# Kernel tuning notes

Hardware: AMD Instinct MI355X
Metric: run time of the kernel (lower is better)

Reference implementation:

```python
import jax, jax.numpy as jnp
import numpy as np

EPS = 1e-12  # matches F.normalize default eps

def _angle(e):
    # e: [N, D] embeddings
    d = e[:, None, :] - e[None, :, :]                      # [N, N, D] pairwise differences
    n = jnp.linalg.norm(d, axis=-1, keepdims=True)         # [N, N, 1]
    d = d / jnp.maximum(n, EPS)                            # normalized diffs; diagonal stays 0
    # all-triplet cosines: for each anchor i, Gram matrix of its normalized diffs
    return jnp.einsum('ijd,ikd->ijk', d, d)                # [N, N, N]

def _smooth_l1_mean(a, b):
    # torch F.smooth_l1_loss with beta=1.0, reduction='mean'
    x = jnp.abs(a - b)
    return jnp.mean(jnp.where(x < 1.0, 0.5 * x * x, x - 0.5))

def setup_inputs() -> dict:
    key = jax.random.key(0)
    k1, k2 = jax.random.split(key)
    student = jax.random.normal(k1, (384, 256), dtype=jnp.float32)
    teacher = jax.random.normal(k2, (384, 256), dtype=jnp.float32)
    return {"student": student, "teacher": teacher}

def reference(student, teacher):
    s_angle = _angle(student)
    t_angle = _angle(teacher)
    return _smooth_l1_mean(s_angle, t_angle)
```

## Files before the change

kernel.cpp:

```cpp
#include <hip/hip_runtime.h>
#include <hip/hip_bf16.h>

#define NPTS 384
#define IT 16
#define NZI (NPTS/IT)
#define DIMS 256

__global__ __launch_bounds__(256) void gram_kernel(
        const float* __restrict__ Es, const float* __restrict__ Et,
        float* __restrict__ Gs, float* __restrict__ Gt,
        float2* __restrict__ UHs, float2* __restrict__ UHt,
        float* __restrict__ out) {
    const int z = blockIdx.z;
    const float* __restrict__ E  = z ? Et : Es;
    float*       __restrict__ G  = z ? Gt : Gs;
    float2*      __restrict__ UH = z ? UHt : UHs;

    const int tx = threadIdx.x;
    const int ty = threadIdx.y;
    const int t  = ty * 16 + tx;
    const int i0 = blockIdx.x * 32;
    const int j0 = blockIdx.y * 32;

    if (blockIdx.x == 0 && blockIdx.y == 0 && z == 0 && t == 0) out[0] = 0.0f;

    __shared__ float sn[64];
    {
        const int r = t >> 2;
        const int p = t & 3;
        const int row = (r < 32) ? (i0 + r) : (j0 + r - 32);
        const float4* __restrict__ src = (const float4*)(E + row * DIMS) + p * 16;
        float s = 0.f;
#pragma unroll
        for (int k = 0; k < 16; k++) {
            float4 v = src[k];
            s += v.x * v.x + v.y * v.y + v.z * v.z + v.w * v.w;
        }
        s += __shfl_xor(s, 1, 64);
        s += __shfl_xor(s, 2, 64);
        if (p == 0) sn[r] = s;
    }
    __syncthreads();

    const int i = i0 + 2 * ty;
    const int j = j0 + 2 * tx;
    const float4* __restrict__ a0 = (const float4*)(E + i * DIMS);
    const float4* __restrict__ a1 = (const float4*)(E + (i + 1) * DIMS);
    const float4* __restrict__ b0 = (const float4*)(E + j * DIMS);
    const float4* __restrict__ b1 = (const float4*)(E + (j + 1) * DIMS);

    float g00 = 0.f, g01 = 0.f, g10 = 0.f, g11 = 0.f;
#pragma unroll 8
    for (int k = 0; k < DIMS / 4; k++) {
        float4 av0 = a0[k], av1 = a1[k], bv0 = b0[k], bv1 = b1[k];
        g00 = fmaf(av0.x, bv0.x, g00); g00 = fmaf(av0.y, bv0.y, g00);
        g00 = fmaf(av0.z, bv0.z, g00); g00 = fmaf(av0.w, bv0.w, g00);
        g01 = fmaf(av0.x, bv1.x, g01); g01 = fmaf(av0.y, bv1.y, g01);
        g01 = fmaf(av0.z, bv1.z, g01); g01 = fmaf(av0.w, bv1.w, g01);
        g10 = fmaf(av1.x, bv0.x, g10); g10 = fmaf(av1.y, bv0.y, g10);
        g10 = fmaf(av1.z, bv0.z, g10); g10 = fmaf(av1.w, bv0.w, g10);
        g11 = fmaf(av1.x, bv1.x, g11); g11 = fmaf(av1.y, bv1.y, g11);
        g11 = fmaf(av1.z, bv1.z, g11); g11 = fmaf(av1.w, bv1.w, g11);
    }

    const float g[2][2] = {{g00, g01}, {g10, g11}};
    const float si[2] = {sn[2 * ty], sn[2 * ty + 1]};
    const float sj[2] = {sn[32 + 2 * tx], sn[32 + 2 * tx + 1]};
#pragma unroll
    for (int r = 0; r < 2; r++) {
#pragma unroll
        for (int c = 0; c < 2; c++) {
            const int ii = i + r, jj = j + c;
            const float gv = g[r][c];
            const float v  = si[r] + sj[c] - 2.0f * gv;
            const float n  = sqrtf(fmaxf(v, 0.0f));
            const float u  = (ii == jj) ? 0.0f : (1.0f / fmaxf(n, 1e-12f));
            G[ii * NPTS + jj]  = gv;
            UH[ii * NPTS + jj] = make_float2(u, 0.5f * si[r] - gv);
        }
    }
}

__global__ __launch_bounds__(256) void rkd_main_kernel(
        const float* __restrict__ Gs, const float* __restrict__ Gt,
        const float2* __restrict__ UHs, const float2* __restrict__ UHt,
        float* __restrict__ out) {
    const int tlin = blockIdx.x;
    const int kt = (int)((sqrtf(8.0f * (float)tlin + 1.0f) - 1.0f) * 0.5f);
    const int jt = tlin - (kt * (kt + 1)) / 2;

    const int tx = threadIdx.x;
    const int ty = threadIdx.y;
    const int jb = jt * 64 + 4 * ty;
    const int kb = kt * 64 + 4 * tx;
    const int ibase = blockIdx.y * IT;

    float wh[4][4];
    const bool offd = (jt != kt);
#pragma unroll
    for (int a = 0; a < 4; a++)
#pragma unroll
        for (int b = 0; b < 4; b++) {
            const int jj = jb + a, kk = kb + b;
            const float w2 = offd ? 2.0f : (kk > jj ? 2.0f : (kk == jj ? 1.0f : 0.0f));
            wh[a][b] = 0.5f * w2;
        }

    float gs[4][4], gt[4][4];
#pragma unroll
    for (int a = 0; a < 4; a++) {
        const float4 vs = *(const float4*)(Gs + (jb + a) * NPTS + kb);
        const float4 vt = *(const float4*)(Gt + (jb + a) * NPTS + kb);
        gs[a][0] = vs.x; gs[a][1] = vs.y; gs[a][2] = vs.z; gs[a][3] = vs.w;
        gt[a][0] = vt.x; gt[a][1] = vt.y; gt[a][2] = vt.z; gt[a][3] = vt.w;
    }

    const float4* __restrict__ pjs = (const float4*)(UHs + (size_t)ibase * NPTS + jb);
    const float4* __restrict__ pjt = (const float4*)(UHt + (size_t)ibase * NPTS + jb);
    const float4* __restrict__ pks = (const float4*)(UHs + (size_t)ibase * NPTS + kb);
    const float4* __restrict__ pkt = (const float4*)(UHt + (size_t)ibase * NPTS + kb);

    float acc = 0.0f;
#pragma unroll 2
    for (int iz = 0; iz < IT; iz++) {
        const int ro = iz * (NPTS / 2);
        const float4 js0 = pjs[ro], js1 = pjs[ro + 1];
        const float4 jt0 = pjt[ro], jt1 = pjt[ro + 1];
        const float4 ks0 = pks[ro], ks1 = pks[ro + 1];
        const float4 kt0 = pkt[ro], kt1 = pkt[ro + 1];

        const float u_sj[4] = {js0.x, js0.z, js1.x, js1.z};
        const float h_sj[4] = {js0.y, js0.w, js1.y, js1.w};
        const float u_tj[4] = {jt0.x, jt0.z, jt1.x, jt1.z};
        const float h_tj[4] = {jt0.y, jt0.w, jt1.y, jt1.w};
        const float u_sk[4] = {ks0.x, ks0.z, ks1.x, ks1.z};
        const float h_sk[4] = {ks0.y, ks0.w, ks1.y, ks1.w};
        const float u_tk[4] = {kt0.x, kt0.z, kt1.x, kt1.z};
        const float h_tk[4] = {kt0.y, kt0.w, kt1.y, kt1.w};

#pragma unroll
        for (int a = 0; a < 4; a++) {
            const float usa = u_sj[a], hsa = h_sj[a];
            const float uta = u_tj[a], hta = h_tj[a];
#pragma unroll
            for (int b = 0; b < 4; b++) {
                const float ts = gs[a][b] + hsa + h_sk[b];
                const float tt = gt[a][b] + hta + h_tk[b];
                const float ps = usa * u_sk[b];
                const float pt = uta * u_tk[b];
                const float mt = pt * tt;
                const float d  = fmaf(ps, ts, -mt);
                const float q  = d * d;
                const float w  = fmaf(2.0f, fabsf(d), -1.0f);
                const float l  = __builtin_amdgcn_fmed3f(q, w, 1.0f);
                acc = fmaf(wh[a][b], l, acc);
            }
        }
    }

#pragma unroll
    for (int off = 32; off > 0; off >>= 1)
        acc += __shfl_down(acc, off, 64);

    __shared__ float wsum[4];
    const int tid  = ty * 16 + tx;
    const int wid  = tid >> 6;
    const int lane = tid & 63;
    if (lane == 0) wsum[wid] = acc;
    __syncthreads();
    if (tid == 0) {
        const float s = wsum[0] + wsum[1] + wsum[2] + wsum[3];
        atomicAdd(out, s * (1.0f / (384.0f * 384.0f * 384.0f)));
    }
}

extern "C" void kernel_launch(void* const* d_in, const int* in_sizes, int n_in,
                              void* d_out, int out_size, void* d_ws, size_t ws_size,
                              hipStream_t stream) {
    const float* student = (const float*)d_in[0];
    const float* teacher = (const float*)d_in[1];
    float* out = (float*)d_out;

    float*  Gs  = (float*)d_ws;
    float*  Gt  = Gs + NPTS * NPTS;
    float2* UHs = (float2*)(Gt + NPTS * NPTS);
    float2* UHt = UHs + NPTS * NPTS;

    gram_kernel<<<dim3(NPTS / 32, NPTS / 32, 2), dim3(16, 16), 0, stream>>>(
        student, teacher, Gs, Gt, UHs, UHt, out);

    rkd_main_kernel<<<dim3(21, NZI), dim3(16, 16), 0, stream>>>(
        Gs, Gt, UHs, UHt, out);
}
```

Baseline: 114.9 us.

## Split Gram computation over K, add derive pass, prefetch and branch main loop

The Gram kernel is split four ways along the feature dimension into partial buffers, and a new elementwise kernel sums the partials and derives norms, inverse distances and half-terms. This raises parallelism in the first stage at the cost of an extra launch and extra workspace traffic. The main kernel halves the i-tile so it launches more blocks, software-prefetches the next row of UH values into registers, and drops the per-element weight multiply on off-diagonal tiles. It also sets occupancy hints through launch_bounds.

New measurement: 109.2 us. -4.9%, faster.

```diff
diff --git a/kernel.cpp b/kernel.cpp
--- a/kernel.cpp
+++ b/kernel.cpp
@@ -2,57 +2,35 @@
 #include <hip/hip_bf16.h>
 
 #define NPTS 384
-#define IT 16
-#define NZI (NPTS/IT)
+#define NN (NPTS * NPTS)
 #define DIMS 256
-
-__global__ __launch_bounds__(256) void gram_kernel(
+#define KSPLIT 4
+#define KCH (DIMS / KSPLIT)
+#define IT 8
+#define NZI (NPTS / IT)
+
+__global__ __launch_bounds__(256, 4) void gram_part_kernel(
         const float* __restrict__ Es, const float* __restrict__ Et,
-        float* __restrict__ Gs, float* __restrict__ Gt,
-        float2* __restrict__ UHs, float2* __restrict__ UHt,
-        float* __restrict__ out) {
-    const int z = blockIdx.z;
-    const float* __restrict__ E  = z ? Et : Es;
-    float*       __restrict__ G  = z ? Gt : Gs;
-    float2*      __restrict__ UH = z ? UHt : UHs;
+        float* __restrict__ P) {
+    const int m  = blockIdx.z >> 2;
+    const int kc = (blockIdx.z & 3) * KCH;
+    const float* __restrict__ E = m ? Et : Es;
+    float* __restrict__ Gp = P + (size_t)blockIdx.z * NN;
 
     const int tx = threadIdx.x;
     const int ty = threadIdx.y;
-    const int t  = ty * 16 + tx;
-    const int i0 = blockIdx.x * 32;
-    const int j0 = blockIdx.y * 32;
-
-    if (blockIdx.x == 0 && blockIdx.y == 0 && z == 0 && t == 0) out[0] = 0.0f;
-
-    __shared__ float sn[64];
-    {
-        const int r = t >> 2;
-        const int p = t & 3;
-        const int row = (r < 32) ? (i0 + r) : (j0 + r - 32);
-        const float4* __restrict__ src = (const float4*)(E + row * DIMS) + p * 16;
-        float s = 0.f;
-#pragma unroll
-        for (int k = 0; k < 16; k++) {
-            float4 v = src[k];
-            s += v.x * v.x + v.y * v.y + v.z * v.z + v.w * v.w;
-        }
-        s += __shfl_xor(s, 1, 64);
-        s += __shfl_xor(s, 2, 64);
-        if (p == 0) sn[r] = s;
-    }
-    __syncthreads();
-
-    const int i = i0 + 2 * ty;
-    const int j = j0 + 2 * tx;
-    const float4* __restrict__ a0 = (const float4*)(E + i * DIMS);
-    const float4* __restrict__ a1 = (const float4*)(E + (i + 1) * DIMS);
-    const float4* __restrict__ b0 = (const float4*)(E + j * DIMS);
-    const float4* __restrict__ b1 = (const float4*)(E + (j + 1) * DIMS);
+    const int i  = blockIdx.x * 32 + 2 * ty;
+    const int j  = blockIdx.y * 32 + 2 * tx;
+
+    const float4* __restrict__ a0 = (const float4*)(E + i * DIMS + kc);
+    const float4* __restrict__ a1 = (const float4*)(E + (i + 1) * DIMS + kc);
+    const float4* __restrict__ b0 = (const float4*)(E + j * DIMS + kc);
+    const float4* __restrict__ b1 = (const float4*)(E + (j + 1) * DIMS + kc);
 
     float g00 = 0.f, g01 = 0.f, g10 = 0.f, g11 = 0.f;
-#pragma unroll 8
-    for (int k = 0; k < DIMS / 4; k++) {
-        float4 av0 = a0[k], av1 = a1[k], bv0 = b0[k], bv1 = b1[k];
+#pragma unroll
+    for (int k = 0; k < KCH / 4; k++) {
+        const float4 av0 = a0[k], av1 = a1[k], bv0 = b0[k], bv1 = b1[k];
         g00 = fmaf(av0.x, bv0.x, g00); g00 = fmaf(av0.y, bv0.y, g00);
         g00 = fmaf(av0.z, bv0.z, g00); g00 = fmaf(av0.w, bv0.w, g00);
         g01 = fmaf(av0.x, bv1.x, g01); g01 = fmaf(av0.y, bv1.y, g01);
@@ -63,25 +41,39 @@
         g11 = fmaf(av1.z, bv1.z, g11); g11 = fmaf(av1.w, bv1.w, g11);
     }
 
-    const float g[2][2] = {{g00, g01}, {g10, g11}};
-    const float si[2] = {sn[2 * ty], sn[2 * ty + 1]};
-    const float sj[2] = {sn[32 + 2 * tx], sn[32 + 2 * tx + 1]};
-#pragma unroll
-    for (int r = 0; r < 2; r++) {
-#pragma unroll
-        for (int c = 0; c < 2; c++) {
-            const int ii = i + r, jj = j + c;
-            const float gv = g[r][c];
-            const float v  = si[r] + sj[c] - 2.0f * gv;
-            const float n  = sqrtf(fmaxf(v, 0.0f));
-            const float u  = (ii == jj) ? 0.0f : (1.0f / fmaxf(n, 1e-12f));
-            G[ii * NPTS + jj]  = gv;
-            UH[ii * NPTS + jj] = make_float2(u, 0.5f * si[r] - gv);
-        }
-    }
-}
-
-__global__ __launch_bounds__(256) void rkd_main_kernel(
+    *(float2*)(Gp + i * NPTS + j)       = make_float2(g00, g01);
+    *(float2*)(Gp + (i + 1) * NPTS + j) = make_float2(g10, g11);
+}
+
+__global__ __launch_bounds__(256, 4) void derive_kernel(
+        const float* __restrict__ P,
+        float* __restrict__ Gs, float* __restrict__ Gt,
+        float2* __restrict__ UHs, float2* __restrict__ UHt,
+        float* __restrict__ out) {
+    const int idx = blockIdx.x * 256 + threadIdx.x;
+    if (idx == 0) out[0] = 0.0f;
+    const int z   = idx / NN;
+    const int rem = idx - z * NN;
+    const int i   = rem / NPTS;
+    const int j   = rem - i * NPTS;
+
+    const float* __restrict__ bz = P + (size_t)z * 4 * NN;
+    const int di = i * (NPTS + 1);
+    const int dj = j * (NPTS + 1);
+
+    const float g   = bz[rem] + bz[NN + rem] + bz[2 * NN + rem] + bz[3 * NN + rem];
+    const float gii = bz[di]  + bz[NN + di]  + bz[2 * NN + di]  + bz[3 * NN + di];
+    const float gjj = bz[dj]  + bz[NN + dj]  + bz[2 * NN + dj]  + bz[3 * NN + dj];
+
+    const float v = gii + gjj - 2.0f * g;
+    const float n = sqrtf(fmaxf(v, 0.0f));
+    const float u = (i == j) ? 0.0f : (1.0f / fmaxf(n, 1e-12f));
+
+    (z ? Gt : Gs)[rem]   = g;
+    (z ? UHt : UHs)[rem] = make_float2(u, 0.5f * gii - g);
+}
+
+__global__ __launch_bounds__(256, 3) void rkd_main_kernel(
         const float* __restrict__ Gs, const float* __restrict__ Gt,
         const float2* __restrict__ UHs, const float2* __restrict__ UHt,
         float* __restrict__ out) {
@@ -95,17 +87,6 @@
     const int kb = kt * 64 + 4 * tx;
     const int ibase = blockIdx.y * IT;
 
-    float wh[4][4];
-    const bool offd = (jt != kt);
-#pragma unroll
-    for (int a = 0; a < 4; a++)
-#pragma unroll
-        for (int b = 0; b < 4; b++) {
-            const int jj = jb + a, kk = kb + b;
-            const float w2 = offd ? 2.0f : (kk > jj ? 2.0f : (kk == jj ? 1.0f : 0.0f));
-            wh[a][b] = 0.5f * w2;
-        }
-
     float gs[4][4], gt[4][4];
 #pragma unroll
     for (int a = 0; a < 4; a++) {
@@ -120,42 +101,83 @@
     const float4* __restrict__ pks = (const float4*)(UHs + (size_t)ibase * NPTS + kb);
     const float4* __restrict__ pkt = (const float4*)(UHt + (size_t)ibase * NPTS + kb);
 
+    const bool offd = (jt != kt);
+    float wh[4][4];
+#pragma unroll
+    for (int a = 0; a < 4; a++)
+#pragma unroll
+        for (int b = 0; b < 4; b++) {
+            const int jj = jb + a, kk = kb + b;
+            wh[a][b] = (kk > jj) ? 1.0f : ((kk == jj) ? 0.5f : 0.0f);
+        }
+
+    float4 L[8];
+    L[0] = pjs[0]; L[1] = pjs[1];
+    L[2] = pjt[0]; L[3] = pjt[1];
+    L[4] = pks[0]; L[5] = pks[1];
+    L[6] = pkt[0]; L[7] = pkt[1];
+
     float acc = 0.0f;
 #pragma unroll 2
     for (int iz = 0; iz < IT; iz++) {
-        const int ro = iz * (NPTS / 2);
-        const float4 js0 = pjs[ro], js1 = pjs[ro + 1];
-        const float4 jt0 = pjt[ro], jt1 = pjt[ro + 1];
-        const float4 ks0 = pks[ro], ks1 = pks[ro + 1];
-        const float4 kt0 = pkt[ro], kt1 = pkt[ro + 1];
-
-        const float u_sj[4] = {js0.x, js0.z, js1.x, js1.z};
-        const float h_sj[4] = {js0.y, js0.w, js1.y, js1.w};
-        const float u_tj[4] = {jt0.x, jt0.z, jt1.x, jt1.z};
-        const float h_tj[4] = {jt0.y, jt0.w, jt1.y, jt1.w};
-        const float u_sk[4] = {ks0.x, ks0.z, ks1.x, ks1.z};
-        const float h_sk[4] = {ks0.y, ks0.w, ks1.y, ks1.w};
-        const float u_tk[4] = {kt0.x, kt0.z, kt1.x, kt1.z};
-        const float h_tk[4] = {kt0.y, kt0.w, kt1.y, kt1.w};
-
-#pragma unroll
-        for (int a = 0; a < 4; a++) {
-            const float usa = u_sj[a], hsa = h_sj[a];
-            const float uta = u_tj[a], hta = h_tj[a];
-#pragma unroll
-            for (int b = 0; b < 4; b++) {
-                const float ts = gs[a][b] + hsa + h_sk[b];
-                const float tt = gt[a][b] + hta + h_tk[b];
-                const float ps = usa * u_sk[b];
-                const float pt = uta * u_tk[b];
-                const float mt = pt * tt;
-                const float d  = fmaf(ps, ts, -mt);
-                const float q  = d * d;
-                const float w  = fmaf(2.0f, fabsf(d), -1.0f);
-                const float l  = __builtin_amdgcn_fmed3f(q, w, 1.0f);
-                acc = fmaf(wh[a][b], l, acc);
+        const int nz = (iz + 1 < IT) ? iz + 1 : iz;
+        const int ro = nz * (NPTS / 2);
+        float4 Ln[8];
+        Ln[0] = pjs[ro];     Ln[1] = pjs[ro + 1];
+        Ln[2] = pjt[ro];     Ln[3] = pjt[ro + 1];
+        Ln[4] = pks[ro];     Ln[5] = pks[ro + 1];
+        Ln[6] = pkt[ro];     Ln[7] = pkt[ro + 1];
+
+        const float u_sj[4] = {L[0].x, L[0].z, L[1].x, L[1].z};
+        const float h_sj[4] = {L[0].y, L[0].w, L[1].y, L[1].w};
+        const float u_tj[4] = {L[2].x, L[2].z, L[3].x, L[3].z};
+        const float h_tj[4] = {L[2].y, L[2].w, L[3].y, L[3].w};
+        const float u_sk[4] = {L[4].x, L[4].z, L[5].x, L[5].z};
+        const float h_sk[4] = {L[4].y, L[4].w, L[5].y, L[5].w};
+        const float u_tk[4] = {L[6].x, L[6].z, L[7].x, L[7].z};
+        const float h_tk[4] = {L[6].y, L[6].w, L[7].y, L[7].w};
+
+        if (offd) {
+#pragma unroll
+            for (int a = 0; a < 4; a++) {
+                const float usa = u_sj[a], hsa = h_sj[a];
+                const float uta = u_tj[a], hta = h_tj[a];
+#pragma unroll
+                for (int b = 0; b < 4; b++) {
+                    const float ts = gs[a][b] + hsa + h_sk[b];
+                    const float tt = gt[a][b] + hta + h_tk[b];
+                    const float ps = usa * u_sk[b];
+                    const float pt = uta * u_tk[b];
+                    const float mt = pt * tt;
+                    const float d  = fmaf(ps, ts, -mt);
+                    const float q  = d * d;
+                    const float w  = fmaf(2.0f, fabsf(d), -1.0f);
+                    acc += __builtin_amdgcn_fmed3f(q, w, 1.0f);
+                }
+            }
+        } else {
+#pragma unroll
+            for (int a = 0; a < 4; a++) {
+                const float usa = u_sj[a], hsa = h_sj[a];
+                const float uta = u_tj[a], hta = h_tj[a];
+#pragma unroll
+                for (int b = 0; b < 4; b++) {
+                    const float ts = gs[a][b] + hsa + h_sk[b];
+                    const float tt = gt[a][b] + hta + h_tk[b];
+                    const float ps = usa * u_sk[b];
+                    const float pt = uta * u_tk[b];
+                    const float mt = pt * tt;
+                    const float d  = fmaf(ps, ts, -mt);
+                    const float q  = d * d;
+                    const float w  = fmaf(2.0f, fabsf(d), -1.0f);
+                    const float l  = __builtin_amdgcn_fmed3f(q, w, 1.0f);
+                    acc = fmaf(wh[a][b], l, acc);
+                }
             }
         }
+
+#pragma unroll
+        for (int r = 0; r < 8; r++) L[r] = Ln[r];
     }
 
 #pragma unroll
@@ -181,13 +203,17 @@
     const float* teacher = (const float*)d_in[1];
     float* out = (float*)d_out;
 
-    float*  Gs  = (float*)d_ws;
-    float*  Gt  = Gs + NPTS * NPTS;
-    float2* UHs = (float2*)(Gt + NPTS * NPTS);
-    float2* UHt = UHs + NPTS * NPTS;
-
-    gram_kernel<<<dim3(NPTS / 32, NPTS / 32, 2), dim3(16, 16), 0, stream>>>(
-        student, teacher, Gs, Gt, UHs, UHt, out);
+    float*  P   = (float*)d_ws;
+    float*  Gs  = P + 8 * NN;
+    float*  Gt  = Gs + NN;
+    float2* UHs = (float2*)(Gt + NN);
+    float2* UHt = UHs + NN;
+
+    gram_part_kernel<<<dim3(NPTS / 32, NPTS / 32, 8), dim3(16, 16), 0, stream>>>(
+        student, teacher, P);
+
+    derive_kernel<<<dim3(2 * NN / 256), 256, 0, stream>>>(
+        P, Gs, Gt, UHs, UHt, out);
 
     rkd_main_kernel<<<dim3(21, NZI), dim3(16, 16), 0, stream>>>(
         Gs, Gt, UHs, UHt, out);
```
